# Optimization experiments

Measured on AMD Instinct MI355X. Metric: run time of the kernel, lower is better.

Reference implementation:

```python
import jax, jax.numpy as jnp
import numpy as np
from jax import lax

WINDOW_SIZE = 11
SIGMA = 1.5
DATA_RANGE = 1.0
LEVELS = 4
EPS = 1e-8
DN = ('NCHW', 'OIHW', 'NCHW')


def _gauss1d(k, sigma):
    coords = jnp.arange(k, dtype=jnp.float32) - k // 2
    g = jnp.exp(-coords ** 2 / (2.0 * sigma ** 2))
    return g / g.sum()


def _blur(x, g):
    # separable depthwise Gaussian blur, VALID padding (use_padding=False)
    C = x.shape[1]
    k = g.shape[0]
    kw = jnp.broadcast_to(g.reshape(1, 1, 1, k), (C, 1, 1, k)).astype(x.dtype)
    kh = jnp.broadcast_to(g.reshape(1, 1, k, 1), (C, 1, k, 1)).astype(x.dtype)
    x = lax.conv_general_dilated(x, kw, (1, 1), 'VALID', dimension_numbers=DN, feature_group_count=C)
    x = lax.conv_general_dilated(x, kh, (1, 1), 'VALID', dimension_numbers=DN, feature_group_count=C)
    return x


def _avg_pool2(x):
    B, C, H, W = x.shape  # H, W even here (512 -> 64)
    return x.reshape(B, C, H // 2, 2, W // 2, 2).mean(axis=(3, 5))


def _ssim_level(X, Y, g):
    C1 = (0.01 * DATA_RANGE) ** 2
    C2 = (0.03 * DATA_RANGE) ** 2
    mu1 = _blur(X, g)
    mu2 = _blur(Y, g)
    sigma1_sq = _blur(X * X, g) - mu1 * mu1
    sigma2_sq = _blur(Y * Y, g) - mu2 * mu2
    sigma12 = _blur(X * Y, g) - mu1 * mu2
    cs_map = jax.nn.relu((2.0 * sigma12 + C2) / (sigma1_sq + sigma2_sq + C2))
    ssim_map = (2.0 * mu1 * mu2 + C1) / (mu1 * mu1 + mu2 * mu2 + C1) * cs_map
    return ssim_map.mean(axis=(1, 2, 3)), cs_map.mean(axis=(1, 2, 3))


def setup_inputs() -> dict:
    key = jax.random.key(0)
    kx, ky = jax.random.split(key)
    X = jax.random.uniform(kx, (16, 3, 512, 512), dtype=jnp.float32)
    Y = jax.random.uniform(ky, (16, 3, 512, 512), dtype=jnp.float32)
    return {'X': X, 'Y': Y}


def reference(X, Y):
    g = _gauss1d(WINDOW_SIZE, SIGMA)
    w = jnp.array([0.0448, 0.2856, 0.3001, 0.2363], dtype=jnp.float32)
    w = w / w.sum()
    vals = []
    for i in range(LEVELS):
        ss, cs = _ssim_level(X, Y, g)
        if i < LEVELS - 1:
            vals.append(cs)
            X = _avg_pool2(X)
            Y = _avg_pool2(Y)
        else:
            vals.append(ss)
    vals = jnp.maximum(jnp.stack(vals, axis=0), EPS)  # [levels, B]
    ms = jnp.prod(vals ** w[:, None], axis=0)
    return 1.0 - ms
```

## Files before the change

kernel.cpp:

```cpp
#include <hip/hip_runtime.h>
#include <math.h>

#define HALO 10
#define TS 32
#define IN 42
#define NP 22
#define XSTR 46
#define HSTR 46
#define NBIN 256

typedef float f2 __attribute__((ext_vector_type(2)));

struct GaussW { float g[11]; };

__global__ void init_acc_kernel(float* P) {
    int i = blockIdx.x * 256 + threadIdx.x;
    if (i < 4 * NBIN * 16) P[i] = 0.f;
}

__global__ __launch_bounds__(256, 4) void ssim_level_kernel(
    const float* __restrict__ X, const float* __restrict__ Y,
    int H, GaussW gw, float* __restrict__ Plevel, int last_level,
    float* __restrict__ Xpool, float* __restrict__ Ypool)
{
    const int W = H;
    const int Hout = H - HALO;

    __shared__ float Xs[IN][XSTR];
    __shared__ float Ys[IN][XSTR];
    __shared__ float Hs[4][TS][HSTR];
    __shared__ float red[4];

    const int tid = threadIdx.x;
    const int bc  = blockIdx.z;
    const int b   = bc / 3;
    const int r0  = blockIdx.y * TS;
    const int c0  = blockIdx.x * TS;
    const size_t base = (size_t)bc * H * W;

    for (int idx = tid; idx < IN * NP; idx += 256) {
        int rr = idx / NP, pp = idx - rr * NP;
        int gr = r0 + rr, gc = c0 + 2 * pp;
        float2 xv = make_float2(0.f, 0.f), yv = make_float2(0.f, 0.f);
        if (gr < H && gc < W) {
            const float* xp = X + base + (size_t)gr * W + gc;
            const float* yp = Y + base + (size_t)gr * W + gc;
            xv = *(const float2*)xp;
            yv = *(const float2*)yp;
        }
        *(float2*)&Xs[rr][2 * pp] = xv;
        *(float2*)&Ys[rr][2 * pp] = yv;
    }
    __syncthreads();

    if (tid < 168) {
        const int rr  = tid >> 2;
        const int seg = tid & 3;
        const int ccb = seg * 8;

        float x[20], y[20];
        #pragma unroll
        for (int u = 0; u < 10; ++u) {
            *(f2*)&x[2 * u] = *(const f2*)&Xs[rr][ccb + 2 * u];
            *(f2*)&y[2 * u] = *(const f2*)&Ys[rr][ccb + 2 * u];
        }

        #pragma unroll
        for (int p = 0; p < 4; ++p) {
            f2 ax = {0.f, 0.f}, ay = {0.f, 0.f};
            #pragma unroll
            for (int k = 0; k < 11; ++k) {
                f2 vx = { x[2 * p + k], x[2 * p + k + 1] };
                f2 vy = { y[2 * p + k], y[2 * p + k + 1] };
                ax += vx * gw.g[k];
                ay += vy * gw.g[k];
            }
            Hs[0][ccb + 2 * p    ][rr] = ax.x;
            Hs[0][ccb + 2 * p + 1][rr] = ax.y;
            Hs[1][ccb + 2 * p    ][rr] = ay.x;
            Hs[1][ccb + 2 * p + 1][rr] = ay.y;
        }
        #pragma unroll
        for (int i = 0; i < 9; ++i) {
            f2 xv = *(f2*)&x[2 * i];
            f2 yv = *(f2*)&y[2 * i];
            f2 a = xv + yv;
            f2 d = xv - yv;
            *(f2*)&x[2 * i] = a * a;
            *(f2*)&y[2 * i] = d * d;
        }
        #pragma unroll
        for (int p = 0; p < 4; ++p) {
            f2 as = {0.f, 0.f}, ad = {0.f, 0.f};
            #pragma unroll
            for (int k = 0; k < 11; ++k) {
                f2 vs = { x[2 * p + k], x[2 * p + k + 1] };
                f2 vd = { y[2 * p + k], y[2 * p + k + 1] };
                as += vs * gw.g[k];
                ad += vd * gw.g[k];
            }
            Hs[2][ccb + 2 * p    ][rr] = as.x;
            Hs[2][ccb + 2 * p + 1][rr] = as.y;
            Hs[3][ccb + 2 * p    ][rr] = ad.x;
            Hs[3][ccb + 2 * p + 1][rr] = ad.y;
        }
    } else if (tid >= 192 && !last_level) {
        const int t = tid - 192;
        const int Wp = W >> 1;
        #pragma unroll
        for (int q = 0; q < 4; ++q) {
            int cell = q * 64 + t;
            int pr = cell >> 4, pc = cell & 15;
            float2 xa = *(const float2*)&Xs[2 * pr][2 * pc];
            float2 xb = *(const float2*)&Xs[2 * pr + 1][2 * pc];
            float2 ya = *(const float2*)&Ys[2 * pr][2 * pc];
            float2 yb = *(const float2*)&Ys[2 * pr + 1][2 * pc];
            size_t o = (size_t)bc * (H >> 1) * Wp + (size_t)(r0 / 2 + pr) * Wp + (c0 / 2 + pc);
            Xpool[o] = 0.25f * (xa.x + xa.y + xb.x + xb.y);
            Ypool[o] = 0.25f * (ya.x + ya.y + yb.x + yb.y);
        }
    }
    __syncthreads();

    const int tx = tid & 31;
    const int ty = tid >> 5;
    const int rb = ty * 4;

    f2 m1[2], m2[2], S[2], D[2];
    #define VPASS(Q, OUT)                                                        \
    {                                                                            \
        float win[14];                                                           \
        _Pragma("unroll")                                                        \
        for (int i = 0; i < 7; ++i)                                              \
            *(f2*)&win[2 * i] = *(const f2*)&Hs[Q][tx][rb + 2 * i];              \
        _Pragma("unroll")                                                        \
        for (int h = 0; h < 2; ++h) {                                            \
            f2 acc = {0.f, 0.f};                                                 \
            _Pragma("unroll")                                                    \
            for (int k = 0; k < 11; ++k) {                                       \
                f2 v = { win[2 * h + k], win[2 * h + k + 1] };                   \
                acc += v * gw.g[k];                                              \
            }                                                                    \
            OUT[h] = acc;                                                        \
        }                                                                        \
    }
    VPASS(0, m1) VPASS(1, m2) VPASS(2, S) VPASS(3, D)
    #undef VPASS

    const float C1 = 1e-4f, C2 = 9e-4f;
    float acc_s = 0.f;
    #pragma unroll
    for (int o = 0; o < 4; ++o) {
        float u1 = m1[o >> 1][o & 1], u2 = m2[o >> 1][o & 1];
        float Sv = S[o >> 1][o & 1],  Dv = D[o >> 1][o & 1];
        float u1s = u1 * u1, u2s = u2 * u2, u12 = u1 * u2;
        float ssum = 0.5f  * (Sv + Dv);
        float sxy  = 0.25f * (Sv - Dv);
        float vsum = ssum - u1s - u2s;
        float v12  = sxy - u12;
        float A2   = fmaxf(2.f * v12 + C2, 0.f);
        float B1   = u1s + u2s + C1;
        float B2   = vsum + C2;
        float inv  = __builtin_amdgcn_rcpf(B1 * B2);
        float val;
        if (!last_level) {
            val = A2 * B1 * inv;
        } else {
            float A1 = 2.f * u12 + C1;
            val = A1 * A2 * inv;
        }
        bool valid = (r0 + rb + o < Hout) && (c0 + tx < Hout);
        acc_s += valid ? val : 0.f;
    }

    #pragma unroll
    for (int off = 32; off; off >>= 1) acc_s += __shfl_down(acc_s, off);
    if ((tid & 63) == 0) red[tid >> 6] = acc_s;
    __syncthreads();
    if (tid == 0) {
        int lin = blockIdx.x + gridDim.x * (blockIdx.y + gridDim.y * blockIdx.z);
        int bin = lin & (NBIN - 1);
        atomicAdd(&Plevel[bin * 16 + b], red[0] + red[1] + red[2] + red[3]);
    }
}

__global__ void finalize_kernel(const float* __restrict__ P, float* __restrict__ out) {
    __shared__ float red[64][4];
    const int tid  = threadIdx.x;
    const int pair = tid >> 2;
    const int chnk = tid & 3;
    const int l = pair >> 4, b = pair & 15;
    float s = 0.f;
    #pragma unroll 4
    for (int j = 0; j < 64; ++j)
        s += P[((l * NBIN) + (chnk * 64) + j) * 16 + b];
    red[pair][chnk] = s;
    __syncthreads();
    if (tid < 16) {
        const int bb = tid;
        const float wraw[4] = {0.0448f, 0.2856f, 0.3001f, 0.2363f};
        float wsum = wraw[0] + wraw[1] + wraw[2] + wraw[3];
        float ms = 1.f;
        for (int ll = 0; ll < 4; ++ll) {
            int Hh = 512 >> ll;
            int Ho = Hh - HALO;
            float cnt = 3.f * (float)Ho * (float)Ho;
            float val = (red[ll * 16 + bb][0] + red[ll * 16 + bb][1] +
                         red[ll * 16 + bb][2] + red[ll * 16 + bb][3]) / cnt;
            val = fmaxf(val, 1e-8f);
            ms *= powf(val, wraw[ll] / wsum);
        }
        out[bb] = 1.f - ms;
    }
}

extern "C" void kernel_launch(void* const* d_in, const int* in_sizes, int n_in,
                              void* d_out, int out_size, void* d_ws, size_t ws_size,
                              hipStream_t stream)
{
    const float* X0 = (const float*)d_in[0];
    const float* Y0 = (const float*)d_in[1];
    float* out = (float*)d_out;
    float* ws  = (float*)d_ws;

    const size_t PSZ = (size_t)4 * NBIN * 16;
    float* P  = ws;
    float* X1 = ws + PSZ;
    float* Y1 = X1 + (size_t)16 * 3 * 256 * 256;
    float* X2 = Y1 + (size_t)16 * 3 * 256 * 256;
    float* Y2 = X2 + (size_t)16 * 3 * 128 * 128;
    float* X3 = Y2 + (size_t)16 * 3 * 128 * 128;
    float* Y3 = X3 + (size_t)16 * 3 * 64 * 64;

    GaussW gw;
    {
        float s = 0.f;
        for (int i = 0; i < 11; ++i) {
            float d = (float)(i - 5);
            gw.g[i] = expf(-d * d / (2.f * 1.5f * 1.5f));
            s += gw.g[i];
        }
        for (int i = 0; i < 11; ++i) gw.g[i] /= s;
    }

    hipLaunchKernelGGL(init_acc_kernel, dim3((4 * NBIN * 16 + 255) / 256), dim3(256), 0, stream, P);

    hipLaunchKernelGGL(ssim_level_kernel, dim3(16, 16, 48), dim3(256), 0, stream,
                       X0, Y0, 512, gw, P + 0 * NBIN * 16, 0, X1, Y1);
    hipLaunchKernelGGL(ssim_level_kernel, dim3(8, 8, 48),   dim3(256), 0, stream,
                       X1, Y1, 256, gw, P + 1 * NBIN * 16, 0, X2, Y2);
    hipLaunchKernelGGL(ssim_level_kernel, dim3(4, 4, 48),   dim3(256), 0, stream,
                       X2, Y2, 128, gw, P + 2 * NBIN * 16, 0, X3, Y3);
    hipLaunchKernelGGL(ssim_level_kernel, dim3(2, 2, 48),   dim3(256), 0, stream,
                       X3, Y3, 64,  gw, P + 3 * NBIN * 16, 1, (float*)nullptr, (float*)nullptr);

    hipLaunchKernelGGL(finalize_kernel, dim3(1), dim3(256), 0, stream, P, out);
}
```

Before: 208.9 us.

## Alias input and horizontal-pass shared buffers to cut LDS and raise occupancy

Merges the X/Y input tiles and the horizontal-blur intermediate into one shared array. Each thread now loads its row window into registers and the block syncs before the intermediate overwrites the input region. The pooling work moves into that earlier phase, the tile load fetches one fewer column pair, and the per-thread window shrinks to 18. Launch bounds go from 4 to 6 blocks per SM and the init kernel is replaced by hipMemsetAsync. This trades an extra barrier and tighter register limits, with a possible spill risk, for lower LDS use and more resident blocks.

```diff
diff --git a/kernel.cpp b/kernel.cpp
--- a/kernel.cpp
+++ b/kernel.cpp
@@ -4,7 +4,7 @@
 #define HALO 10
 #define TS 32
 #define IN 42
-#define NP 22
+#define NP 21
 #define XSTR 46
 #define HSTR 46
 #define NBIN 256
@@ -13,12 +13,8 @@
 
 struct GaussW { float g[11]; };
 
-__global__ void init_acc_kernel(float* P) {
-    int i = blockIdx.x * 256 + threadIdx.x;
-    if (i < 4 * NBIN * 16) P[i] = 0.f;
-}
-
-__global__ __launch_bounds__(256, 4) void ssim_level_kernel(
+
+__global__ __launch_bounds__(256, 6) void ssim_level_kernel(
     const float* __restrict__ X, const float* __restrict__ Y,
     int H, GaussW gw, float* __restrict__ Plevel, int last_level,
     float* __restrict__ Xpool, float* __restrict__ Ypool)
@@ -26,10 +22,10 @@
     const int W = H;
     const int Hout = H - HALO;
 
-    __shared__ float Xs[IN][XSTR];
-    __shared__ float Ys[IN][XSTR];
-    __shared__ float Hs[4][TS][HSTR];
+    __shared__ float U[4 * TS * HSTR];
     __shared__ float red[4];
+    float* Xs = U;
+    float* Ys = U + IN * XSTR;
 
     const int tid = threadIdx.x;
     const int bc  = blockIdx.z;
@@ -48,23 +44,40 @@
             xv = *(const float2*)xp;
             yv = *(const float2*)yp;
         }
-        *(float2*)&Xs[rr][2 * pp] = xv;
-        *(float2*)&Ys[rr][2 * pp] = yv;
-    }
-    __syncthreads();
-
+        *(float2*)&Xs[rr * XSTR + 2 * pp] = xv;
+        *(float2*)&Ys[rr * XSTR + 2 * pp] = yv;
+    }
+    __syncthreads();
+
+    float x[18], y[18];
+    int rr = 0, ccb = 0;
     if (tid < 168) {
-        const int rr  = tid >> 2;
-        const int seg = tid & 3;
-        const int ccb = seg * 8;
-
-        float x[20], y[20];
-        #pragma unroll
-        for (int u = 0; u < 10; ++u) {
-            *(f2*)&x[2 * u] = *(const f2*)&Xs[rr][ccb + 2 * u];
-            *(f2*)&y[2 * u] = *(const f2*)&Ys[rr][ccb + 2 * u];
-        }
-
+        rr  = tid >> 2;
+        ccb = (tid & 3) * 8;
+        #pragma unroll
+        for (int u = 0; u < 9; ++u) {
+            *(f2*)&x[2 * u] = *(const f2*)&Xs[rr * XSTR + ccb + 2 * u];
+            *(f2*)&y[2 * u] = *(const f2*)&Ys[rr * XSTR + ccb + 2 * u];
+        }
+    } else if (tid >= 192 && !last_level) {
+        const int t = tid - 192;
+        const int Wp = W >> 1;
+        #pragma unroll
+        for (int q = 0; q < 4; ++q) {
+            int cell = q * 64 + t;
+            int pr = cell >> 4, pc = cell & 15;
+            float2 xa = *(const float2*)&Xs[(2 * pr)     * XSTR + 2 * pc];
+            float2 xb = *(const float2*)&Xs[(2 * pr + 1) * XSTR + 2 * pc];
+            float2 ya = *(const float2*)&Ys[(2 * pr)     * XSTR + 2 * pc];
+            float2 yb = *(const float2*)&Ys[(2 * pr + 1) * XSTR + 2 * pc];
+            size_t o = (size_t)bc * (H >> 1) * Wp + (size_t)(r0 / 2 + pr) * Wp + (c0 / 2 + pc);
+            Xpool[o] = 0.25f * (xa.x + xa.y + xb.x + xb.y);
+            Ypool[o] = 0.25f * (ya.x + ya.y + yb.x + yb.y);
+        }
+    }
+    __syncthreads();
+
+    if (tid < 168) {
         #pragma unroll
         for (int p = 0; p < 4; ++p) {
             f2 ax = {0.f, 0.f}, ay = {0.f, 0.f};
@@ -75,10 +88,10 @@
                 ax += vx * gw.g[k];
                 ay += vy * gw.g[k];
             }
-            Hs[0][ccb + 2 * p    ][rr] = ax.x;
-            Hs[0][ccb + 2 * p + 1][rr] = ax.y;
-            Hs[1][ccb + 2 * p    ][rr] = ay.x;
-            Hs[1][ccb + 2 * p + 1][rr] = ay.y;
+            U[(0 * TS + ccb + 2 * p    ) * HSTR + rr] = ax.x;
+            U[(0 * TS + ccb + 2 * p + 1) * HSTR + rr] = ax.y;
+            U[(1 * TS + ccb + 2 * p    ) * HSTR + rr] = ay.x;
+            U[(1 * TS + ccb + 2 * p + 1) * HSTR + rr] = ay.y;
         }
         #pragma unroll
         for (int i = 0; i < 9; ++i) {
@@ -99,25 +112,10 @@
                 as += vs * gw.g[k];
                 ad += vd * gw.g[k];
             }
-            Hs[2][ccb + 2 * p    ][rr] = as.x;
-            Hs[2][ccb + 2 * p + 1][rr] = as.y;
-            Hs[3][ccb + 2 * p    ][rr] = ad.x;
-            Hs[3][ccb + 2 * p + 1][rr] = ad.y;
-        }
-    } else if (tid >= 192 && !last_level) {
-        const int t = tid - 192;
-        const int Wp = W >> 1;
-        #pragma unroll
-        for (int q = 0; q < 4; ++q) {
-            int cell = q * 64 + t;
-            int pr = cell >> 4, pc = cell & 15;
-            float2 xa = *(const float2*)&Xs[2 * pr][2 * pc];
-            float2 xb = *(const float2*)&Xs[2 * pr + 1][2 * pc];
-            float2 ya = *(const float2*)&Ys[2 * pr][2 * pc];
-            float2 yb = *(const float2*)&Ys[2 * pr + 1][2 * pc];
-            size_t o = (size_t)bc * (H >> 1) * Wp + (size_t)(r0 / 2 + pr) * Wp + (c0 / 2 + pc);
-            Xpool[o] = 0.25f * (xa.x + xa.y + xb.x + xb.y);
-            Ypool[o] = 0.25f * (ya.x + ya.y + yb.x + yb.y);
+            U[(2 * TS + ccb + 2 * p    ) * HSTR + rr] = as.x;
+            U[(2 * TS + ccb + 2 * p + 1) * HSTR + rr] = as.y;
+            U[(3 * TS + ccb + 2 * p    ) * HSTR + rr] = ad.x;
+            U[(3 * TS + ccb + 2 * p + 1) * HSTR + rr] = ad.y;
         }
     }
     __syncthreads();
@@ -132,7 +130,7 @@
         float win[14];                                                           \
         _Pragma("unroll")                                                        \
         for (int i = 0; i < 7; ++i)                                              \
-            *(f2*)&win[2 * i] = *(const f2*)&Hs[Q][tx][rb + 2 * i];              \
+            *(f2*)&win[2 * i] = *(const f2*)&U[(Q * TS + tx) * HSTR + rb + 2 * i]; \
         _Pragma("unroll")                                                        \
         for (int h = 0; h < 2; ++h) {                                            \
             f2 acc = {0.f, 0.f};                                                 \
@@ -243,7 +241,7 @@
         for (int i = 0; i < 11; ++i) gw.g[i] /= s;
     }
 
-    hipLaunchKernelGGL(init_acc_kernel, dim3((4 * NBIN * 16 + 255) / 256), dim3(256), 0, stream, P);
+    hipMemsetAsync(P, 0, PSZ * sizeof(float), stream);
 
     hipLaunchKernelGGL(ssim_level_kernel, dim3(16, 16, 48), dim3(256), 0, stream,
                        X0, Y0, 512, gw, P + 0 * NBIN * 16, 0, X1, Y1);
```

New measurement: 201.0 us. -3.8%, faster.
